# Performance work log

Measured on AMD Instinct MI355X. Metric: run time of the kernel, lower is better.

The kernel has to match this reference:

```python
import jax, jax.numpy as jnp
import numpy as np

D_MODEL = 256
N_HEADS_SA = 8
CA_HEADS = 8
CA_DH = 64
CA_INNER = CA_HEADS * CA_DH  # 512
N_POINTS = 4
D_FFN = 1024
OFFSET_SCALE = 2.0
B, NQ = 4, 1024
T, H, W = 4, 64, 64
LV = T * H * W

PNAMES = ['sa_Wq','sa_bq','sa_Wk','sa_bk','sa_Wv','sa_bv','sa_Wo','sa_bo',
          'ln1_g','ln1_b','ln2_g','ln2_b','ln3_g','ln3_b',
          'ca_Wq','ca_bq','ca_Wk','ca_bk','ca_Wv','ca_bv','ca_Wref','ca_bref',
          'ca_Woff','ca_boff','ca_Wo','ca_bo',
          'ffn_W1','ffn_b1','ffn_W2','ffn_b2']


def _layer_norm(x, g, b, eps=1e-5):
    m = x.mean(-1, keepdims=True)
    v = ((x - m) ** 2).mean(-1, keepdims=True)
    return (x - m) * jax.lax.rsqrt(v + eps) * g + b


def _mha(q, k, v, Wq, bq, Wk, bk, Wv, bv, Wo, bo, n_heads):
    Bq, N, D = q.shape
    dh = D // n_heads
    scale = 1.0 / float(np.sqrt(dh))
    qh = (q @ Wq + bq).reshape(Bq, N, n_heads, dh)
    kh = (k @ Wk + bk).reshape(Bq, N, n_heads, dh)
    vh = (v @ Wv + bv).reshape(Bq, N, n_heads, dh)
    attn = jax.nn.softmax(jnp.einsum('bqhd,bkhd->bhqk', qh, kh) * scale, -1)
    out = jnp.einsum('bhqk,bkhd->bqhd', attn, vh).reshape(Bq, N, D)
    return out @ Wo + bo


def _trilinear_sample(vol, loc, sizes_f):
    # vol: [B, L, Hd, dh] flattened (T*H*W) volume per head
    # loc: [B, N, Hd, P, 3] normalized (t, h, w) coords in [0, 1]
    Bv, L, Hd, dh = vol.shape
    _, N, _, P, _ = loc.shape
    pos = jnp.clip(loc, 0.0, 1.0) * (sizes_f - 1.0)  # align_corners voxel coords
    p0 = jnp.floor(pos)
    frac = pos - p0
    p0i = p0.astype(jnp.int32)
    sizes_i = sizes_f.astype(jnp.int32)
    Hn, Wn = sizes_i[1], sizes_i[2]
    vol_t = vol.transpose(0, 2, 1, 3)  # [B, Hd, L, dh]
    out = jnp.zeros((Bv, Hd, N * P, dh), vol.dtype)
    for dt in (0, 1):
        for dy in (0, 1):
            for dx in (0, 1):
                c = jnp.minimum(p0i + jnp.array([dt, dy, dx], jnp.int32), sizes_i - 1)
                wt = (frac[..., 0] if dt else 1.0 - frac[..., 0]) \
                   * (frac[..., 1] if dy else 1.0 - frac[..., 1]) \
                   * (frac[..., 2] if dx else 1.0 - frac[..., 2])  # [B,N,Hd,P]
                idx = c[..., 0] * (Hn * Wn) + c[..., 1] * Wn + c[..., 2]
                idx_t = idx.transpose(0, 2, 1, 3).reshape(Bv, Hd, N * P, 1)
                g = jnp.take_along_axis(vol_t, idx_t, axis=2)  # [B,Hd,N*P,dh]
                w_t = wt.transpose(0, 2, 1, 3).reshape(Bv, Hd, N * P, 1)
                out = out + g * w_t
    return out.reshape(Bv, Hd, N, P, dh).transpose(0, 2, 1, 3, 4)  # [B,N,Hd,P,dh]


def _deform_cross_attn(query, key, value, flow_key, flow_value, spatial_shapes, p):
    Bq, N, _ = query.shape
    L = key.shape[1]
    sizes_f = spatial_shapes[0].astype(jnp.float32)  # single level (T, H, W)
    qh = (query @ p['ca_Wq'] + p['ca_bq']).reshape(Bq, N, CA_HEADS, CA_DH)
    ref = jax.nn.sigmoid(query @ p['ca_Wref'] + p['ca_bref'])  # [B,N,3]
    off = (query @ p['ca_Woff'] + p['ca_boff']).reshape(Bq, N, CA_HEADS, N_POINTS, 3)
    loc = ref[:, :, None, None, :] + off * (OFFSET_SCALE / sizes_f)
    k_vol = (key @ p['ca_Wk'] + p['ca_bk']).reshape(Bq, L, CA_HEADS, CA_DH)
    v_vol = (value @ p['ca_Wv'] + p['ca_bv']).reshape(Bq, L, CA_HEADS, CA_DH)
    fk_vol = (flow_key @ p['ca_Wk'] + p['ca_bk']).reshape(Bq, L, CA_HEADS, CA_DH)
    fv_vol = (flow_value @ p['ca_Wv'] + p['ca_bv']).reshape(Bq, L, CA_HEADS, CA_DH)
    k_s = _trilinear_sample(k_vol, loc, sizes_f)
    v_s = _trilinear_sample(v_vol, loc, sizes_f)
    fk_s = _trilinear_sample(fk_vol, loc, sizes_f)
    fv_s = _trilinear_sample(fv_vol, loc, sizes_f)
    scale = 1.0 / float(np.sqrt(CA_DH))
    logits = jnp.concatenate([
        jnp.einsum('bnhd,bnhpd->bnhp', qh, k_s),
        jnp.einsum('bnhd,bnhpd->bnhp', qh, fk_s)], -1) * scale
    attn = jax.nn.softmax(logits, -1)  # joint softmax over image+flow sampled points
    vals = jnp.concatenate([v_s, fv_s], 3)  # [B,N,Hd,2P,dh]
    out = jnp.einsum('bnhp,bnhpd->bnhd', attn, vals).reshape(Bq, N, CA_INNER)
    return out @ p['ca_Wo'] + p['ca_bo']


def _forward(query, query_pos, img, flow, pos_emb, spatial_shapes, p):
    q = query + query_pos
    sa = _mha(q, q, query, p['sa_Wq'], p['sa_bq'], p['sa_Wk'], p['sa_bk'],
              p['sa_Wv'], p['sa_bv'], p['sa_Wo'], p['sa_bo'], N_HEADS_SA)
    x = _layer_norm(query + sa, p['ln1_g'], p['ln1_b'])
    key = pos_emb + img
    flow_key = pos_emb + flow
    ca = _deform_cross_attn(x, key, img, flow_key, flow, spatial_shapes, p)
    x = _layer_norm(x + ca, p['ln2_g'], p['ln2_b'])
    ffn = jax.nn.relu(x @ p['ffn_W1'] + p['ffn_b1']) @ p['ffn_W2'] + p['ffn_b2']
    return _layer_norm(x + ffn, p['ln3_g'], p['ln3_b'])


def setup_inputs() -> dict:
    key = jax.random.key(0)
    ks = iter(jax.random.split(key, 64))
    def rn(shape, s=1.0):
        return jax.random.normal(next(ks), shape, jnp.float32) * s
    inp = {
        'query': rn((B, NQ, D_MODEL)),
        'query_pos': rn((B, NQ, D_MODEL)),
        'img_embed_flatten': rn((B, LV, D_MODEL)),
        'flow_embed_flatten': rn((B, LV, D_MODEL)),
        'indicator_temporal_lvl_pos_embed_flatten': rn((B, LV, D_MODEL)),
        'spatial_shapes': jnp.array([[T, H, W]], jnp.int32),
    }
    for nm in ['sa_Wq', 'sa_Wk', 'sa_Wv', 'sa_Wo']:
        inp[nm] = rn((D_MODEL, D_MODEL), 0.02)
    for nm in ['sa_bq', 'sa_bk', 'sa_bv', 'sa_bo', 'ln1_b', 'ln2_b', 'ln3_b']:
        inp[nm] = jnp.zeros((D_MODEL,), jnp.float32)
    for nm in ['ln1_g', 'ln2_g', 'ln3_g']:
        inp[nm] = jnp.ones((D_MODEL,), jnp.float32)
    inp['ca_Wq'] = rn((D_MODEL, CA_INNER), 0.02); inp['ca_bq'] = jnp.zeros((CA_INNER,), jnp.float32)
    inp['ca_Wk'] = rn((D_MODEL, CA_INNER), 0.02); inp['ca_bk'] = jnp.zeros((CA_INNER,), jnp.float32)
    inp['ca_Wv'] = rn((D_MODEL, CA_INNER), 0.02); inp['ca_bv'] = jnp.zeros((CA_INNER,), jnp.float32)
    inp['ca_Wref'] = rn((D_MODEL, 3), 0.02); inp['ca_bref'] = jnp.zeros((3,), jnp.float32)
    inp['ca_Woff'] = rn((D_MODEL, CA_HEADS * N_POINTS * 3), 0.02)
    inp['ca_boff'] = jnp.zeros((CA_HEADS * N_POINTS * 3,), jnp.float32)
    inp['ca_Wo'] = rn((CA_INNER, D_MODEL), 0.02); inp['ca_bo'] = jnp.zeros((D_MODEL,), jnp.float32)
    inp['ffn_W1'] = rn((D_MODEL, D_FFN), 0.02); inp['ffn_b1'] = jnp.zeros((D_FFN,), jnp.float32)
    inp['ffn_W2'] = rn((D_FFN, D_MODEL), 0.02); inp['ffn_b2'] = jnp.zeros((D_MODEL,), jnp.float32)
    return inp


def reference(query, query_pos, img_embed_flatten, flow_embed_flatten,
              indicator_temporal_lvl_pos_embed_flatten, spatial_shapes,
              sa_Wq, sa_bq, sa_Wk, sa_bk, sa_Wv, sa_bv, sa_Wo, sa_bo,
              ln1_g, ln1_b, ln2_g, ln2_b, ln3_g, ln3_b,
              ca_Wq, ca_bq, ca_Wk, ca_bk, ca_Wv, ca_bv, ca_Wref, ca_bref,
              ca_Woff, ca_boff, ca_Wo, ca_bo,
              ffn_W1, ffn_b1, ffn_W2, ffn_b2):
    p = dict(zip(PNAMES, (sa_Wq, sa_bq, sa_Wk, sa_bk, sa_Wv, sa_bv, sa_Wo, sa_bo,
                          ln1_g, ln1_b, ln2_g, ln2_b, ln3_g, ln3_b,
                          ca_Wq, ca_bq, ca_Wk, ca_bk, ca_Wv, ca_bv, ca_Wref, ca_bref,
                          ca_Woff, ca_boff, ca_Wo, ca_bo,
                          ffn_W1, ffn_b1, ffn_W2, ffn_b2)))
    return _forward(query, query_pos, img_embed_flatten, flow_embed_flatten,
                    indicator_temporal_lvl_pos_embed_flatten, spatial_shapes, p)
```

## Files before the change

### kernel.cpp

```cpp
#include <hip/hip_runtime.h>
#include <hip/hip_bf16.h>

#define BQ 4
#define NQT 1024
#define DM 256
#define HSA 8
#define DHSA 32
#define CAH 8
#define CADH 64
#define CAI 512
#define NPT 4
#define DFFN 1024
#define TT 4
#define HH 64
#define WW 64
#define LVOL 16384

using bf16 = __hip_bfloat16;
typedef __attribute__((ext_vector_type(4))) float fx4;
typedef __attribute__((ext_vector_type(8))) short s8v;
typedef __attribute__((ext_vector_type(4))) short s4v;

__device__ __forceinline__ float b2f(bf16 v) { return __bfloat162float(v); }
__device__ __forceinline__ bf16  f2b(float v) { return __float2bfloat16(v); }
__device__ __forceinline__ short f2bs(float v) {
  bf16 b = __float2bfloat16(v);
  return *reinterpret_cast<short*>(&b);
}

__device__ __forceinline__ float wave_sum64(float v) {
#pragma unroll
  for (int o = 32; o >= 1; o >>= 1) v += __shfl_xor(v, o, 64);
  return v;
}

__device__ __forceinline__ s8v pack8(float4 a, float4 b) {
  return (s8v){f2bs(a.x), f2bs(a.y), f2bs(a.z), f2bs(a.w),
               f2bs(b.x), f2bs(b.y), f2bs(b.z), f2bs(b.w)};
}

__device__ __forceinline__ void gl_lds16(const void* g, void* l) {
  __builtin_amdgcn_global_load_lds(
      (const __attribute__((address_space(1))) unsigned int*)g,
      (__attribute__((address_space(3))) unsigned int*)l, 16, 0, 0);
}

template <int KSH>
__global__ __launch_bounds__(256) void wtrans_k(const float* __restrict__ W,
                                               short* __restrict__ Wt, int N) {
  const int i = blockIdx.x * 256 + threadIdx.x;
  const int k = i & ((1 << KSH) - 1);
  const int n = i >> KSH;
  Wt[i] = f2bs(W[(size_t)k * N + n]);
}

template <int DUAL>
__global__ __launch_bounds__(256) void prep_k(const float* __restrict__ A,
                                              const float* __restrict__ B,
                                              short* __restrict__ O, int n8) {
  for (int i = blockIdx.x * 256 + threadIdx.x; i < n8; i += gridDim.x * 256) {
    float4 a0 = *(const float4*)&A[(size_t)i * 8];
    float4 a1 = *(const float4*)&A[(size_t)i * 8 + 4];
    if (DUAL) {
      const float4 b0 = *(const float4*)&B[(size_t)i * 8];
      const float4 b1 = *(const float4*)&B[(size_t)i * 8 + 4];
      a0.x += b0.x; a0.y += b0.y; a0.z += b0.z; a0.w += b0.w;
      a1.x += b1.x; a1.y += b1.y; a1.z += b1.z; a1.w += b1.w;
    }
    *(s8v*)&O[(size_t)i * 8] = pack8(a0, a1);
  }
}

__global__ __launch_bounds__(256) void bgemm_k(
    const short* __restrict__ A, const short* __restrict__ Wt,
    const float* __restrict__ bias, bf16* __restrict__ Cout,
    int M, int N, int K) {
  __shared__ short As[2][128 * 32];
  __shared__ short Bs[2][128 * 32];
  const int tid = threadIdx.x;
  const int lane = tid & 63, w = tid >> 6;
  const int wr = w >> 1, wc = w & 1;
  const int lm = lane & 15, quad = lane >> 4;
  const int nwg = gridDim.x * gridDim.y;
  const int ib = blockIdx.y * gridDim.x + blockIdx.x;
  const int id = (ib & 7) * (nwg >> 3) + (ib >> 3);
  const int m0 = (id / gridDim.x) * 128;
  const int n0 = (id % gridDim.x) * 128;

  const int srow = lane >> 2;
  const int scol = (lane & 3) * 8;
  const size_t arow = (size_t)(m0 + w * 32 + srow);
  const size_t brow = (size_t)(n0 + w * 32 + srow);

  fx4 acc[4][4] = {};
  const int nt = K / 32;
  int cur = 0;
  {
    gl_lds16(&A[arow * K + scol], &As[0][(w * 32) * 32]);
    gl_lds16(&A[(arow + 16) * K + scol], &As[0][(w * 32 + 16) * 32]);
    gl_lds16(&Wt[brow * K + scol], &Bs[0][(w * 32) * 32]);
    gl_lds16(&Wt[(brow + 16) * K + scol], &Bs[0][(w * 32 + 16) * 32]);
  }
  __syncthreads();
  for (int t = 0; t < nt; t++) {
    if (t + 1 < nt) {
      const int k0 = (t + 1) * 32;
      gl_lds16(&A[arow * K + k0 + scol], &As[cur ^ 1][(w * 32) * 32]);
      gl_lds16(&A[(arow + 16) * K + k0 + scol], &As[cur ^ 1][(w * 32 + 16) * 32]);
      gl_lds16(&Wt[brow * K + k0 + scol], &Bs[cur ^ 1][(w * 32) * 32]);
      gl_lds16(&Wt[(brow + 16) * K + k0 + scol], &Bs[cur ^ 1][(w * 32 + 16) * 32]);
    }
    s8v af[4], bfr[4];
#pragma unroll
    for (int f = 0; f < 4; f++) {
      af[f] = *(s8v*)&As[cur][(wr * 64 + f * 16 + lm) * 32 + quad * 8];
      bfr[f] = *(s8v*)&Bs[cur][(wc * 64 + f * 16 + lm) * 32 + quad * 8];
    }
#pragma unroll
    for (int fm = 0; fm < 4; fm++)
#pragma unroll
      for (int fn = 0; fn < 4; fn++)
        acc[fm][fn] = __builtin_amdgcn_mfma_f32_16x16x32_bf16(
            af[fm], bfr[fn], acc[fm][fn], 0, 0, 0);
    __syncthreads();
    cur ^= 1;
  }
#pragma unroll
  for (int fn = 0; fn < 4; fn++) {
    const int n = n0 + wc * 64 + fn * 16 + lm;
    const float bb = bias[n];
#pragma unroll
    for (int fm = 0; fm < 4; fm++) {
      const int mbase = m0 + wr * 64 + fm * 16 + quad * 4;
#pragma unroll
      for (int r = 0; r < 4; r++)
        Cout[(size_t)(mbase + r) * N + n] = f2b(acc[fm][fn][r] + bb);
    }
  }
}

template <int DUAL, int RELU, int OUTBF>
__global__ __launch_bounds__(256) void mgemm_k(
    const float* __restrict__ A, const float* __restrict__ A2,
    const short* __restrict__ Wt, const float* __restrict__ bias,
    void* __restrict__ Cout, int M, int N, int K) {
  __shared__ short As[2][128 * 40];
  __shared__ short Bs[2][128 * 40];
  const int tid = threadIdx.x;
  const int lane = tid & 63, w = tid >> 6;
  const int wr = w >> 1, wc = w & 1;
  const int lm = lane & 15, quad = lane >> 4;
  const int nwg = gridDim.x * gridDim.y;
  const int ib = blockIdx.y * gridDim.x + blockIdx.x;
  const int id = (ib & 7) * (nwg >> 3) + (ib >> 3);
  const int m0 = (id / gridDim.x) * 128;
  const int n0 = (id % gridDim.x) * 128;

  const int am = tid >> 3, ak = (tid & 7) * 4;

  float4 pa[4], pa2[4];
  s8v pb[2];
  auto loadT = [&](int k0) {
#pragma unroll
    for (int i = 0; i < 4; i++) {
      pa[i] = *(const float4*)&A[(size_t)(m0 + am + i * 32) * K + k0 + ak];
      if (DUAL)
        pa2[i] = *(const float4*)&A2[(size_t)(m0 + am + i * 32) * K + k0 + ak];
    }
#pragma unroll
    for (int i = 0; i < 2; i++) {
      int unit = tid + i * 256;
      pb[i] = *(const s8v*)&Wt[(size_t)(n0 + (unit >> 2)) * K + k0 +
                               (unit & 3) * 8];
    }
  };
  auto stageT = [&](int buf) {
#pragma unroll
    for (int i = 0; i < 4; i++) {
      float x0 = pa[i].x, x1 = pa[i].y, x2 = pa[i].z, x3 = pa[i].w;
      if (DUAL) { x0 += pa2[i].x; x1 += pa2[i].y; x2 += pa2[i].z; x3 += pa2[i].w; }
      s4v sv = {f2bs(x0), f2bs(x1), f2bs(x2), f2bs(x3)};
      *(s4v*)&As[buf][(am + i * 32) * 40 + ak] = sv;
    }
#pragma unroll
    for (int i = 0; i < 2; i++) {
      int unit = tid + i * 256;
      *(s8v*)&Bs[buf][(unit >> 2) * 40 + (unit & 3) * 8] = pb[i];
    }
  };

  fx4 acc[4][4] = {};
  loadT(0);
  stageT(0);
  __syncthreads();
  int cur = 0;
  for (int k0 = 0; k0 < K; k0 += 32) {
    const int more = (k0 + 32 < K);
    if (more) loadT(k0 + 32);
    s8v af[4], bfr[4];
#pragma unroll
    for (int f = 0; f < 4; f++) {
      af[f] = *(s8v*)&As[cur][(wr * 64 + f * 16 + lm) * 40 + quad * 8];
      bfr[f] = *(s8v*)&Bs[cur][(wc * 64 + f * 16 + lm) * 40 + quad * 8];
    }
#pragma unroll
    for (int fm = 0; fm < 4; fm++)
#pragma unroll
      for (int fn = 0; fn < 4; fn++)
        acc[fm][fn] = __builtin_amdgcn_mfma_f32_16x16x32_bf16(
            af[fm], bfr[fn], acc[fm][fn], 0, 0, 0);
    if (more) stageT(cur ^ 1);
    __syncthreads();
    cur ^= 1;
  }
#pragma unroll
  for (int fn = 0; fn < 4; fn++) {
    const int n = n0 + wc * 64 + fn * 16 + lm;
    const float bb = bias[n];
#pragma unroll
    for (int fm = 0; fm < 4; fm++) {
      const int mbase = m0 + wr * 64 + fm * 16 + quad * 4;
#pragma unroll
      for (int r = 0; r < 4; r++) {
        float v = acc[fm][fn][r] + bb;
        if (RELU) v = fmaxf(v, 0.0f);
        const size_t off = (size_t)(mbase + r) * N + n;
        if (OUTBF)
          ((bf16*)Cout)[off] = f2b(v);
        else
          ((float*)Cout)[off] = v;
      }
    }
  }
}

__global__ __launch_bounds__(256) void sa_flash_k(
    const float* __restrict__ qh, const float* __restrict__ kh,
    const float* __restrict__ vh, float* __restrict__ outp) {
  __shared__ short Ks[64 * 72];
  __shared__ short Vt[32 * 72];
  __shared__ short Ps[64 * 72];
  const int qt = blockIdx.x, h = blockIdx.y, b = blockIdx.z;
  const int tid = threadIdx.x;
  const int w = tid >> 6, lane = tid & 63;
  const int lm = lane & 15, quad = lane >> 4;
  const size_t rowbase = (size_t)(b * NQT) * DM + h * DHSA;

  s8v aq;
  {
    const int qrow = qt * 64 + w * 16 + lm;
    const float* qp = &qh[rowbase + (size_t)qrow * DM + quad * 8];
    const float4 q0 = *(const float4*)qp;
    const float4 q1 = *(const float4*)(qp + 4);
    const float sc = 0.17677669529663687f;
    aq = (s8v){f2bs(q0.x * sc), f2bs(q0.y * sc), f2bs(q0.z * sc), f2bs(q0.w * sc),
               f2bs(q1.x * sc), f2bs(q1.y * sc), f2bs(q1.z * sc), f2bs(q1.w * sc)};
  }

  fx4 o0 = {}, o1 = {};
  float mrun[4] = {-1e30f, -1e30f, -1e30f, -1e30f};
  float lrun[4] = {0.f, 0.f, 0.f, 0.f};
  const int jr = tid >> 2;
  const int d0 = (tid & 3) * 8;

  for (int jt = 0; jt < 16; jt++) {
    __syncthreads();
    {
      const size_t rb = rowbase + (size_t)(jt * 64 + jr) * DM + d0;
      const float4 k0 = *(const float4*)&kh[rb];
      const float4 k1 = *(const float4*)&kh[rb + 4];
      *(s8v*)&Ks[jr * 72 + d0] = pack8(k0, k1);
      const float4 v0 = *(const float4*)&vh[rb];
      const float4 v1 = *(const float4*)&vh[rb + 4];
      Vt[(d0 + 0) * 72 + jr] = f2bs(v0.x);
      Vt[(d0 + 1) * 72 + jr] = f2bs(v0.y);
      Vt[(d0 + 2) * 72 + jr] = f2bs(v0.z);
      Vt[(d0 + 3) * 72 + jr] = f2bs(v0.w);
      Vt[(d0 + 4) * 72 + jr] = f2bs(v1.x);
      Vt[(d0 + 5) * 72 + jr] = f2bs(v1.y);
      Vt[(d0 + 6) * 72 + jr] = f2bs(v1.z);
      Vt[(d0 + 7) * 72 + jr] = f2bs(v1.w);
    }
    __syncthreads();
    fx4 s[4];
    const fx4 zero = {};
#pragma unroll
    for (int nf = 0; nf < 4; nf++) {
      s8v kb = *(const s8v*)&Ks[(nf * 16 + lm) * 72 + quad * 8];
      s[nf] = __builtin_amdgcn_mfma_f32_16x16x32_bf16(aq, kb, zero, 0, 0, 0);
    }
#pragma unroll
    for (int r = 0; r < 4; r++) {
      float mx = fmaxf(fmaxf(s[0][r], s[1][r]), fmaxf(s[2][r], s[3][r]));
#pragma unroll
      for (int off = 8; off >= 1; off >>= 1)
        mx = fmaxf(mx, __shfl_xor(mx, off, 64));
      const float mnew = fmaxf(mrun[r], mx);
      const float corr = expf(mrun[r] - mnew);
      mrun[r] = mnew;
      float p0 = expf(s[0][r] - mnew);
      float p1 = expf(s[1][r] - mnew);
      float p2 = expf(s[2][r] - mnew);
      float p3 = expf(s[3][r] - mnew);
      float rs = p0 + p1 + p2 + p3;
#pragma unroll
      for (int off = 8; off >= 1; off >>= 1) rs += __shfl_xor(rs, off, 64);
      lrun[r] = lrun[r] * corr + rs;
      o0[r] *= corr;
      o1[r] *= corr;
      s[0][r] = p0; s[1][r] = p1; s[2][r] = p2; s[3][r] = p3;
    }
#pragma unroll
    for (int nf = 0; nf < 4; nf++)
#pragma unroll
      for (int r = 0; r < 4; r++)
        Ps[(w * 16 + quad * 4 + r) * 72 + nf * 16 + lm] = f2bs(s[nf][r]);
#pragma unroll
    for (int ks = 0; ks < 2; ks++) {
      s8v pf = *(const s8v*)&Ps[(w * 16 + lm) * 72 + ks * 32 + quad * 8];
      s8v vb0 = *(const s8v*)&Vt[lm * 72 + ks * 32 + quad * 8];
      s8v vb1 = *(const s8v*)&Vt[(16 + lm) * 72 + ks * 32 + quad * 8];
      o0 = __builtin_amdgcn_mfma_f32_16x16x32_bf16(pf, vb0, o0, 0, 0, 0);
      o1 = __builtin_amdgcn_mfma_f32_16x16x32_bf16(pf, vb1, o1, 0, 0, 0);
    }
  }
#pragma unroll
  for (int r = 0; r < 4; r++) {
    const float inv = 1.0f / lrun[r];
    const size_t base =
        rowbase + (size_t)(qt * 64 + w * 16 + quad * 4 + r) * DM;
    outp[base + lm] = o0[r] * inv;
    outp[base + 16 + lm] = o1[r] * inv;
  }
}

__global__ __launch_bounds__(128) void refoff_k(
    const float* __restrict__ x1, const float* __restrict__ Wref,
    const float* __restrict__ bref, const float* __restrict__ Woff,
    const float* __restrict__ boff, float* __restrict__ refb,
    float* __restrict__ offb) {
  __shared__ float xs[256];
  const int row = blockIdx.x;
  const int tid = threadIdx.x;
  xs[tid] = x1[(size_t)row * DM + tid];
  xs[tid + 128] = x1[(size_t)row * DM + tid + 128];
  __syncthreads();
  if (tid < 3) {
    float s = bref[tid];
    for (int d = 0; d < 256; d++) s = fmaf(xs[d], Wref[d * 3 + tid], s);
    refb[(size_t)row * 3 + tid] = 1.0f / (1.0f + expf(-s));
  } else if (tid < 99) {
    int o = tid - 3;
    float s = boff[o];
    for (int d = 0; d < 256; d++) s = fmaf(xs[d], Woff[d * 96 + o], s);
    offb[(size_t)row * 96 + o] = s;
  }
}

__device__ __forceinline__ void calc_corners(
    const float* __restrict__ refb, const float* __restrict__ offb, int bn,
    int h, int (&idxs)[NPT][8], float (&wts)[NPT][8]) {
  const float rt = refb[bn * 3 + 0], ry = refb[bn * 3 + 1], rx = refb[bn * 3 + 2];
  const float* ofp = &offb[(size_t)bn * 96 + h * 12];
#pragma unroll
  for (int p = 0; p < NPT; p++) {
    float lt = rt + ofp[p * 3 + 0] * 0.5f;
    float ly = ry + ofp[p * 3 + 1] * 0.03125f;
    float lx = rx + ofp[p * 3 + 2] * 0.03125f;
    float pt = fminf(fmaxf(lt, 0.f), 1.f) * (TT - 1);
    float py = fminf(fmaxf(ly, 0.f), 1.f) * (HH - 1);
    float px = fminf(fmaxf(lx, 0.f), 1.f) * (WW - 1);
    float f0t = floorf(pt), f0y = floorf(py), f0x = floorf(px);
    float frt = pt - f0t, fry = py - f0y, frx = px - f0x;
    int t0 = (int)f0t, y0 = (int)f0y, x0 = (int)f0x;
    int t1 = min(t0 + 1, TT - 1), y1 = min(y0 + 1, HH - 1), x1 = min(x0 + 1, WW - 1);
    float wt0 = 1.f - frt, wy0 = 1.f - fry, wx0 = 1.f - frx;
#pragma unroll
    for (int c = 0; c < 8; c++) {
      int dt = c >> 2, dy = (c >> 1) & 1, dx = c & 1;
      int ct = dt ? t1 : t0, cy = dy ? y1 : y0, cx = dx ? x1 : x0;
      idxs[p][c] = ct * (HH * WW) + cy * WW + cx;
      wts[p][c] = (dt ? frt : wt0) * (dy ? fry : wy0) * (dx ? frx : wx0);
    }
  }
}

__global__ __launch_bounds__(256) void ca_logits_k(
    const float* __restrict__ qh, const float* __restrict__ refb,
    const float* __restrict__ offb, const bf16* __restrict__ vol,
    float* __restrict__ logits, int slot) {
  const int wid = (blockIdx.x * blockDim.x + threadIdx.x) >> 6;
  const int lane = threadIdx.x & 63;
  const int h = wid & 7;
  const int bn = wid >> 3;
  const int b = bn >> 10;
  const float q = qh[(size_t)bn * CAI + h * CADH + lane];
  int idxs[NPT][8];
  float wts[NPT][8];
  calc_corners(refb, offb, bn, h, idxs, wts);
  const size_t volbase = (size_t)b * LVOL * CAI + h * CADH + lane;
  float* lp = logits + ((size_t)bn * CAH + h) * 8 + slot;
#pragma unroll
  for (int p = 0; p < NPT; p++) {
    float ks = 0.f;
#pragma unroll
    for (int c = 0; c < 8; c++)
      ks = fmaf(wts[p][c], b2f(vol[volbase + (size_t)idxs[p][c] * CAI]), ks);
    float li = wave_sum64(q * ks) * 0.125f;
    if (lane == p) lp[p] = li;
  }
}

__global__ __launch_bounds__(256) void ca_softmax_k(float* __restrict__ logits) {
  const int i = blockIdx.x * blockDim.x + threadIdx.x;
  float* p = logits + (size_t)i * 8;
  float v[8], m = -1e30f;
#pragma unroll
  for (int j = 0; j < 8; j++) { v[j] = p[j]; m = fmaxf(m, v[j]); }
  float s = 0.f;
#pragma unroll
  for (int j = 0; j < 8; j++) { v[j] = expf(v[j] - m); s += v[j]; }
  const float inv = 1.0f / s;
#pragma unroll
  for (int j = 0; j < 8; j++) p[j] = v[j] * inv;
}

template <int FIRST>
__global__ __launch_bounds__(256) void ca_acc_k(
    const float* __restrict__ refb, const float* __restrict__ offb,
    const bf16* __restrict__ vol, const float* __restrict__ attn,
    float* __restrict__ acc, int slot) {
  const int wid = (blockIdx.x * blockDim.x + threadIdx.x) >> 6;
  const int lane = threadIdx.x & 63;
  const int h = wid & 7;
  const int bn = wid >> 3;
  const int b = bn >> 10;
  int idxs[NPT][8];
  float wts[NPT][8];
  calc_corners(refb, offb, bn, h, idxs, wts);
  const size_t volbase = (size_t)b * LVOL * CAI + h * CADH + lane;
  const float* ap = attn + ((size_t)bn * CAH + h) * 8 + slot;
  const size_t off = (size_t)bn * CAI + h * CADH + lane;
  float a = FIRST ? 0.f : acc[off];
#pragma unroll
  for (int p = 0; p < NPT; p++) {
    float vs = 0.f;
#pragma unroll
    for (int c = 0; c < 8; c++)
      vs = fmaf(wts[p][c], b2f(vol[volbase + (size_t)idxs[p][c] * CAI]), vs);
    a = fmaf(ap[p], vs, a);
  }
  acc[off] = a;
}

__global__ __launch_bounds__(256) void ln_k(
    const float* __restrict__ resv, const float* __restrict__ x,
    const float* __restrict__ g, const float* __restrict__ bb,
    float* __restrict__ of) {
  const int row = (blockIdx.x * blockDim.x + threadIdx.x) >> 6;
  const int lane = threadIdx.x & 63;
  const size_t base = (size_t)row * DM;
  float v[4];
#pragma unroll
  for (int i = 0; i < 4; i++) {
    int d = lane + i * 64;
    v[i] = resv[base + d] + x[base + d];
  }
  float s = wave_sum64(v[0] + v[1] + v[2] + v[3]);
  const float mean = s * (1.0f / 256.0f);
  float vs = 0.f;
#pragma unroll
  for (int i = 0; i < 4; i++) { float d0 = v[i] - mean; vs = fmaf(d0, d0, vs); }
  vs = wave_sum64(vs);
  const float rstd = rsqrtf(vs * (1.0f / 256.0f) + 1e-5f);
#pragma unroll
  for (int i = 0; i < 4; i++) {
    int d = lane + i * 64;
    of[base + d] = (v[i] - mean) * rstd * g[d] + bb[d];
  }
}

extern "C" void kernel_launch(void* const* d_in, const int* in_sizes, int n_in,
                              void* d_out, int out_size, void* d_ws,
                              size_t ws_size, hipStream_t stream) {
  const float* query = (const float*)d_in[0];
  const float* qpos = (const float*)d_in[1];
  const float* img = (const float*)d_in[2];
  const float* flow = (const float*)d_in[3];
  const float* pos = (const float*)d_in[4];
  const float* sa_Wq = (const float*)d_in[6];
  const float* sa_Wk = (const float*)d_in[7];
  const float* sa_Wv = (const float*)d_in[8];
  const float* sa_Wo = (const float*)d_in[9];
  const float* sa_bq = (const float*)d_in[10];
  const float* sa_bk = (const float*)d_in[11];
  const float* sa_bv = (const float*)d_in[12];
  const float* sa_bo = (const float*)d_in[13];
  const float* ln1_b = (const float*)d_in[14];
  const float* ln2_b = (const float*)d_in[15];
  const float* ln3_b = (const float*)d_in[16];
  const float* ln1_g = (const float*)d_in[17];
  const float* ln2_g = (const float*)d_in[18];
  const float* ln3_g = (const float*)d_in[19];
  const float* ca_Wq = (const float*)d_in[20];
  const float* ca_bq = (const float*)d_in[21];
  const float* ca_Wk = (const float*)d_in[22];
  const float* ca_bk = (const float*)d_in[23];
  const float* ca_Wv = (const float*)d_in[24];
  const float* ca_bv = (const float*)d_in[25];
  const float* ca_Wref = (const float*)d_in[26];
  const float* ca_bref = (const float*)d_in[27];
  const float* ca_Woff = (const float*)d_in[28];
  const float* ca_boff = (const float*)d_in[29];
  const float* ca_Wo = (const float*)d_in[30];
  const float* ca_bo = (const float*)d_in[31];
  const float* ffn_W1 = (const float*)d_in[32];
  const float* ffn_b1 = (const float*)d_in[33];
  const float* ffn_W2 = (const float*)d_in[34];
  const float* ffn_b2 = (const float*)d_in[35];

  const int MQ = BQ * NQT;
  const int MV = BQ * LVOL;
  const size_t MB = 1024 * 1024;

  char* r0 = (char*)d_ws;
  char* w = r0 + 64 * MB;
  auto alloc = [&](size_t n) {
    char* p = w;
    w += (n + 255) & ~(size_t)255;
    return p;
  };
  float* x1_f = (float*)alloc((size_t)MQ * DM * 4);
  float* ca_qh = (float*)alloc((size_t)MQ * CAI * 4);
  float* refb = (float*)alloc((size_t)MQ * 3 * 4);
  float* offb = (float*)alloc((size_t)MQ * 96 * 4);
  float* logits = (float*)alloc((size_t)MQ * CAH * 8 * 4);
  float* ca_acc = (float*)alloc((size_t)MQ * CAI * 4);
  short* WtsaQ = (short*)alloc((size_t)DM * DM * 2);
  short* WtsaK = (short*)alloc((size_t)DM * DM * 2);
  short* WtsaV = (short*)alloc((size_t)DM * DM * 2);
  short* WtsaO = (short*)alloc((size_t)DM * DM * 2);
  short* Wtcaq = (short*)alloc((size_t)CAI * DM * 2);
  short* Wtk = (short*)alloc((size_t)CAI * DM * 2);
  short* Wtv = (short*)alloc((size_t)CAI * DM * 2);
  short* Wtcao = (short*)alloc((size_t)DM * CAI * 2);
  short* Wtf1 = (short*)alloc((size_t)DFFN * DM * 2);
  short* Wtf2 = (short*)alloc((size_t)DM * DFFN * 2);
  short* abuf = (short*)alloc((size_t)MV * DM * 2);
  if ((size_t)(w - (char*)d_ws) > ws_size) return;

  float* qh_sa = (float*)(r0 + 0 * MB);
  float* kh_sa = (float*)(r0 + 4 * MB);
  float* vh_sa = (float*)(r0 + 8 * MB);
  float* sa_att = (float*)(r0 + 12 * MB);
  float* sa_proj = (float*)(r0 + 16 * MB);
  bf16* vol = (bf16*)r0;
  float* ca_o = (float*)(r0 + 0 * MB);
  float* x2_f = (float*)(r0 + 4 * MB);
  float* ffn_h = (float*)(r0 + 8 * MB);
  float* ffn_o = (float*)(r0 + 24 * MB);

  const int n8v = MV * DM / 8;

  dim3 blk(256);
  wtrans_k<8><<<dim3(DM * DM / 256), blk, 0, stream>>>(sa_Wq, WtsaQ, DM);
  wtrans_k<8><<<dim3(DM * DM / 256), blk, 0, stream>>>(sa_Wk, WtsaK, DM);
  wtrans_k<8><<<dim3(DM * DM / 256), blk, 0, stream>>>(sa_Wv, WtsaV, DM);
  wtrans_k<8><<<dim3(DM * DM / 256), blk, 0, stream>>>(sa_Wo, WtsaO, DM);
  wtrans_k<8><<<dim3(DM * CAI / 256), blk, 0, stream>>>(ca_Wq, Wtcaq, CAI);
  wtrans_k<8><<<dim3(DM * CAI / 256), blk, 0, stream>>>(ca_Wk, Wtk, CAI);
  wtrans_k<8><<<dim3(DM * CAI / 256), blk, 0, stream>>>(ca_Wv, Wtv, CAI);
  wtrans_k<8><<<dim3(DM * DFFN / 256), blk, 0, stream>>>(ffn_W1, Wtf1, DFFN);
  wtrans_k<9><<<dim3(CAI * DM / 256), blk, 0, stream>>>(ca_Wo, Wtcao, DM);
  wtrans_k<10><<<dim3(DFFN * DM / 256), blk, 0, stream>>>(ffn_W2, Wtf2, DM);
  mgemm_k<1, 0, 0><<<dim3(DM / 128, MQ / 128), blk, 0, stream>>>(query, qpos, WtsaQ, sa_bq, (void*)qh_sa, MQ, DM, DM);
  mgemm_k<1, 0, 0><<<dim3(DM / 128, MQ / 128), blk, 0, stream>>>(query, qpos, WtsaK, sa_bk, (void*)kh_sa, MQ, DM, DM);
  mgemm_k<0, 0, 0><<<dim3(DM / 128, MQ / 128), blk, 0, stream>>>(query, query, WtsaV, sa_bv, (void*)vh_sa, MQ, DM, DM);
  sa_flash_k<<<dim3(16, 8, 4), blk, 0, stream>>>(qh_sa, kh_sa, vh_sa, sa_att);
  mgemm_k<0, 0, 0><<<dim3(DM / 128, MQ / 128), blk, 0, stream>>>(sa_att, sa_att, WtsaO, sa_bo, (void*)sa_proj, MQ, DM, DM);
  ln_k<<<dim3(MQ / 4), blk, 0, stream>>>(query, sa_proj, ln1_g, ln1_b, x1_f);
  mgemm_k<0, 0, 0><<<dim3(CAI / 128, MQ / 128), blk, 0, stream>>>(x1_f, x1_f, Wtcaq, ca_bq, (void*)ca_qh, MQ, CAI, DM);
  refoff_k<<<dim3(MQ), dim3(128), 0, stream>>>(x1_f, ca_Wref, ca_bref, ca_Woff, ca_boff, refb, offb);
  prep_k<1><<<dim3(2048), blk, 0, stream>>>(pos, img, abuf, n8v);
  bgemm_k<<<dim3(CAI / 128, MV / 128), blk, 0, stream>>>(abuf, Wtk, ca_bk, vol, MV, CAI, DM);
  ca_logits_k<<<dim3(8192), blk, 0, stream>>>(ca_qh, refb, offb, vol, logits, 0);
  prep_k<1><<<dim3(2048), blk, 0, stream>>>(pos, flow, abuf, n8v);
  bgemm_k<<<dim3(CAI / 128, MV / 128), blk, 0, stream>>>(abuf, Wtk, ca_bk, vol, MV, CAI, DM);
  ca_logits_k<<<dim3(8192), blk, 0, stream>>>(ca_qh, refb, offb, vol, logits, 4);
  ca_softmax_k<<<dim3(128), blk, 0, stream>>>(logits);
  prep_k<0><<<dim3(2048), blk, 0, stream>>>(img, img, abuf, n8v);
  bgemm_k<<<dim3(CAI / 128, MV / 128), blk, 0, stream>>>(abuf, Wtv, ca_bv, vol, MV, CAI, DM);
  ca_acc_k<1><<<dim3(8192), blk, 0, stream>>>(refb, offb, vol, logits, ca_acc, 0);
  prep_k<0><<<dim3(2048), blk, 0, stream>>>(flow, flow, abuf, n8v);
  bgemm_k<<<dim3(CAI / 128, MV / 128), blk, 0, stream>>>(abuf, Wtv, ca_bv, vol, MV, CAI, DM);
  ca_acc_k<0><<<dim3(8192), blk, 0, stream>>>(refb, offb, vol, logits, ca_acc, 4);
  mgemm_k<0, 0, 0><<<dim3(DM / 128, MQ / 128), blk, 0, stream>>>(ca_acc, ca_acc, Wtcao, ca_bo, (void*)ca_o, MQ, DM, CAI);
  ln_k<<<dim3(MQ / 4), blk, 0, stream>>>(x1_f, ca_o, ln2_g, ln2_b, x2_f);
  mgemm_k<0, 1, 0><<<dim3(DFFN / 128, MQ / 128), blk, 0, stream>>>(x2_f, x2_f, Wtf1, ffn_b1, (void*)ffn_h, MQ, DFFN, DM);
  mgemm_k<0, 0, 0><<<dim3(DM / 128, MQ / 128), blk, 0, stream>>>(ffn_h, ffn_h, Wtf2, ffn_b2, (void*)ffn_o, MQ, DM, DFFN);
  ln_k<<<dim3(MQ / 4), blk, 0, stream>>>(x2_f, ffn_o, ln3_g, ln3_b, (float*)d_out);
}
```

Before: 725.1 us.

## Split self-attention keys across two blocks with merge kernel; narrow prep_k vectors

```diff
diff --git a/kernel.cpp b/kernel.cpp
--- a/kernel.cpp
+++ b/kernel.cpp
@@ -57,17 +57,15 @@
 template <int DUAL>
 __global__ __launch_bounds__(256) void prep_k(const float* __restrict__ A,
                                               const float* __restrict__ B,
-                                              short* __restrict__ O, int n8) {
-  for (int i = blockIdx.x * 256 + threadIdx.x; i < n8; i += gridDim.x * 256) {
-    float4 a0 = *(const float4*)&A[(size_t)i * 8];
-    float4 a1 = *(const float4*)&A[(size_t)i * 8 + 4];
+                                              short* __restrict__ O, int n4) {
+  const int stride = gridDim.x * 256;
+  for (int i = blockIdx.x * 256 + threadIdx.x; i < n4; i += stride) {
+    float4 a = ((const float4*)A)[i];
     if (DUAL) {
-      const float4 b0 = *(const float4*)&B[(size_t)i * 8];
-      const float4 b1 = *(const float4*)&B[(size_t)i * 8 + 4];
-      a0.x += b0.x; a0.y += b0.y; a0.z += b0.z; a0.w += b0.w;
-      a1.x += b1.x; a1.y += b1.y; a1.z += b1.z; a1.w += b1.w;
-    }
-    *(s8v*)&O[(size_t)i * 8] = pack8(a0, a1);
+      const float4 b = ((const float4*)B)[i];
+      a.x += b.x; a.y += b.y; a.z += b.z; a.w += b.w;
+    }
+    ((s4v*)O)[i] = (s4v){f2bs(a.x), f2bs(a.y), f2bs(a.z), f2bs(a.w)};
   }
 }
 
@@ -236,15 +234,19 @@
 
 __global__ __launch_bounds__(256) void sa_flash_k(
     const float* __restrict__ qh, const float* __restrict__ kh,
-    const float* __restrict__ vh, float* __restrict__ outp) {
+    const float* __restrict__ vh, float* __restrict__ op0,
+    float* __restrict__ op1, float* __restrict__ mlb) {
   __shared__ short Ks[64 * 72];
   __shared__ short Vt[32 * 72];
   __shared__ short Ps[64 * 72];
-  const int qt = blockIdx.x, h = blockIdx.y, b = blockIdx.z;
+  const int qt = blockIdx.x, h = blockIdx.y;
+  const int b = blockIdx.z >> 1, half = blockIdx.z & 1;
   const int tid = threadIdx.x;
   const int w = tid >> 6, lane = tid & 63;
   const int lm = lane & 15, quad = lane >> 4;
   const size_t rowbase = (size_t)(b * NQT) * DM + h * DHSA;
+  float* __restrict__ opart = half ? op1 : op0;
+  float* __restrict__ ml = mlb + (size_t)half * (32768 * 2);
 
   s8v aq;
   {
@@ -263,7 +265,7 @@
   const int jr = tid >> 2;
   const int d0 = (tid & 3) * 8;
 
-  for (int jt = 0; jt < 16; jt++) {
+  for (int jt = half * 8; jt < half * 8 + 8; jt++) {
     __syncthreads();
     {
       const size_t rb = rowbase + (size_t)(jt * 64 + jr) * DM + d0;
@@ -326,12 +328,33 @@
   }
 #pragma unroll
   for (int r = 0; r < 4; r++) {
-    const float inv = 1.0f / lrun[r];
-    const size_t base =
-        rowbase + (size_t)(qt * 64 + w * 16 + quad * 4 + r) * DM;
-    outp[base + lm] = o0[r] * inv;
-    outp[base + 16 + lm] = o1[r] * inv;
-  }
+    const int row = qt * 64 + w * 16 + quad * 4 + r;
+    const size_t base = rowbase + (size_t)row * DM;
+    opart[base + lm] = o0[r];
+    opart[base + 16 + lm] = o1[r];
+    if (lm == 0) {
+      const int rowid = (b * 8 + h) * 1024 + row;
+      ml[(size_t)rowid * 2] = mrun[r];
+      ml[(size_t)rowid * 2 + 1] = lrun[r];
+    }
+  }
+}
+
+__global__ __launch_bounds__(256) void sa_merge_k(
+    const float* __restrict__ op0, const float* __restrict__ op1,
+    const float* __restrict__ mlb, float* __restrict__ outp) {
+  const int t = blockIdx.x * 256 + threadIdx.x;
+  const int d = t & 31;
+  const int rowid = t >> 5;
+  const int n = rowid & 1023, h = (rowid >> 10) & 7, b = rowid >> 13;
+  const size_t addr = ((size_t)(b * NQT + n)) * DM + h * DHSA + d;
+  const float m0 = mlb[(size_t)rowid * 2], l0 = mlb[(size_t)rowid * 2 + 1];
+  const float m1 = mlb[65536 + (size_t)rowid * 2];
+  const float l1 = mlb[65536 + (size_t)rowid * 2 + 1];
+  const float M = fmaxf(m0, m1);
+  const float w0 = expf(m0 - M), w1 = expf(m1 - M);
+  const float inv = 1.0f / (l0 * w0 + l1 * w1);
+  outp[addr] = (op0[addr] * w0 + op1[addr] * w1) * inv;
 }
 
 __global__ __launch_bounds__(128) void refoff_k(
@@ -554,13 +577,16 @@
   float* vh_sa = (float*)(r0 + 8 * MB);
   float* sa_att = (float*)(r0 + 12 * MB);
   float* sa_proj = (float*)(r0 + 16 * MB);
+  float* o_p0 = (float*)(r0 + 20 * MB);
+  float* o_p1 = (float*)(r0 + 24 * MB);
+  float* mlb = (float*)(r0 + 28 * MB);
   bf16* vol = (bf16*)r0;
   float* ca_o = (float*)(r0 + 0 * MB);
   float* x2_f = (float*)(r0 + 4 * MB);
   float* ffn_h = (float*)(r0 + 8 * MB);
   float* ffn_o = (float*)(r0 + 24 * MB);
 
-  const int n8v = MV * DM / 8;
+  const int n4v = MV * DM / 4;
 
   dim3 blk(256);
   wtrans_k<8><<<dim3(DM * DM / 256), blk, 0, stream>>>(sa_Wq, WtsaQ, DM);
@@ -576,22 +602,23 @@
   mgemm_k<1, 0, 0><<<dim3(DM / 128, MQ / 128), blk, 0, stream>>>(query, qpos, WtsaQ, sa_bq, (void*)qh_sa, MQ, DM, DM);
   mgemm_k<1, 0, 0><<<dim3(DM / 128, MQ / 128), blk, 0, stream>>>(query, qpos, WtsaK, sa_bk, (void*)kh_sa, MQ, DM, DM);
   mgemm_k<0, 0, 0><<<dim3(DM / 128, MQ / 128), blk, 0, stream>>>(query, query, WtsaV, sa_bv, (void*)vh_sa, MQ, DM, DM);
-  sa_flash_k<<<dim3(16, 8, 4), blk, 0, stream>>>(qh_sa, kh_sa, vh_sa, sa_att);
+  sa_flash_k<<<dim3(16, 8, 8), blk, 0, stream>>>(qh_sa, kh_sa, vh_sa, o_p0, o_p1, mlb);
+  sa_merge_k<<<dim3(4096), blk, 0, stream>>>(o_p0, o_p1, mlb, sa_att);
   mgemm_k<0, 0, 0><<<dim3(DM / 128, MQ / 128), blk, 0, stream>>>(sa_att, sa_att, WtsaO, sa_bo, (void*)sa_proj, MQ, DM, DM);
   ln_k<<<dim3(MQ / 4), blk, 0, stream>>>(query, sa_proj, ln1_g, ln1_b, x1_f);
   mgemm_k<0, 0, 0><<<dim3(CAI / 128, MQ / 128), blk, 0, stream>>>(x1_f, x1_f, Wtcaq, ca_bq, (void*)ca_qh, MQ, CAI, DM);
   refoff_k<<<dim3(MQ), dim3(128), 0, stream>>>(x1_f, ca_Wref, ca_bref, ca_Woff, ca_boff, refb, offb);
-  prep_k<1><<<dim3(2048), blk, 0, stream>>>(pos, img, abuf, n8v);
+  prep_k<1><<<dim3(2048), blk, 0, stream>>>(pos, img, abuf, n4v);
   bgemm_k<<<dim3(CAI / 128, MV / 128), blk, 0, stream>>>(abuf, Wtk, ca_bk, vol, MV, CAI, DM);
   ca_logits_k<<<dim3(8192), blk, 0, stream>>>(ca_qh, refb, offb, vol, logits, 0);
-  prep_k<1><<<dim3(2048), blk, 0, stream>>>(pos, flow, abuf, n8v);
+  prep_k<1><<<dim3(2048), blk, 0, stream>>>(pos, flow, abuf, n4v);
   bgemm_k<<<dim3(CAI / 128, MV / 128), blk, 0, stream>>>(abuf, Wtk, ca_bk, vol, MV, CAI, DM);
   ca_logits_k<<<dim3(8192), blk, 0, stream>>>(ca_qh, refb, offb, vol, logits, 4);
   ca_softmax_k<<<dim3(128), blk, 0, stream>>>(logits);
-  prep_k<0><<<dim3(2048), blk, 0, stream>>>(img, img, abuf, n8v);
+  prep_k<0><<<dim3(2048), blk, 0, stream>>>(img, img, abuf, n4v);
   bgemm_k<<<dim3(CAI / 128, MV / 128), blk, 0, stream>>>(abuf, Wtv, ca_bv, vol, MV, CAI, DM);
   ca_acc_k<1><<<dim3(8192), blk, 0, stream>>>(refb, offb, vol, logits, ca_acc, 0);
-  prep_k<0><<<dim3(2048), blk, 0, stream>>>(flow, flow, abuf, n8v);
+  prep_k<0><<<dim3(2048), blk, 0, stream>>>(flow, flow, abuf, n4v);
   bgemm_k<<<dim3(CAI / 128, MV / 128), blk, 0, stream>>>(abuf, Wtv, ca_bv, vol, MV, CAI, DM);
   ca_acc_k<0><<<dim3(8192), blk, 0, stream>>>(refb, offb, vol, logits, ca_acc, 4);
   mgemm_k<0, 0, 0><<<dim3(DM / 128, MQ / 128), blk, 0, stream>>>(ca_acc, ca_acc, Wtcao, ca_bo, (void*)ca_o, MQ, DM, CAI);
```

Result: no change. 728.5 us (+0.5%).
